# Performance work log

Measured on AMD Instinct MI355X. Metric: run time of the kernel, lower is better.

The kernel has to match this reference:

```python
import jax, jax.numpy as jnp
import numpy as np

# Segment geometry (from init_kwargs): modes ['u','uv','v'] -> out_v = alpha * x_u @ W_uv
U = 128
V = 128
IN_OFF = [0, 128, 256, 384]
W_OFF = [k * U * V for k in range(8)]          # [0,16384,...,114688]
OUT_OFF = [0, 128, 256, 384]
IN_STRIDE = 512
OUT_STRIDE = 512
W_STRIDE = 8 * U * V                           # 131072
# (in_seg, w_seg, out_seg, coefficient)
PATHS = [(0, 0, 0, 1.0), (1, 1, 1, 1.0), (2, 2, 2, 1.0), (3, 3, 3, 1.0),
         (0, 4, 1, 0.5), (1, 5, 2, 0.5), (2, 6, 3, 0.5), (3, 7, 0, 0.5)]
B = 32768
E = 4  # num_embeddings (experts)


def setup_inputs() -> dict:
    key = jax.random.key(0)
    k1, k2, k3 = jax.random.split(key, 3)
    tensor_in = jax.random.normal(k1, (B, IN_STRIDE), dtype=jnp.float32)
    tensor_w = jax.random.normal(k2, (E, W_STRIDE), dtype=jnp.float32)
    tensor_w_id = jax.random.randint(k3, (B,), 0, E, dtype=jnp.int32)
    return {"tensor_in": tensor_in, "tensor_w": tensor_w, "tensor_w_id": tensor_w_id}


def _batch_linear(tensor_in, tensor_w, tensor_w_id):
    """Segmented path-indexed grouped linear (cuEquivariance BatchLinear fwd).

    tensor_in: [B, IN_STRIDE]; tensor_w: [E, W_STRIDE]; tensor_w_id: [B] int in [0,E).
    For each path (i, j, k, alpha):
        out[b, OUT_OFF[k]:+V] += alpha * x[b, IN_OFF[i]:+U] @ W[w_id[b], seg j].reshape(U, V)
    """
    nb = tensor_in.shape[0]
    ne = tensor_w.shape[0]
    onehot = jax.nn.one_hot(tensor_w_id, ne, dtype=tensor_in.dtype)  # [B, E]
    out = jnp.zeros((nb, OUT_STRIDE), dtype=tensor_in.dtype)
    for (i, j, k, a) in PATHS:
        x = tensor_in[:, IN_OFF[i]:IN_OFF[i] + U]                    # [B, U]
        w_seg = tensor_w[:, W_OFF[j]:W_OFF[j] + U * V].reshape(ne, U, V)
        # masked per-expert dense GEMMs (small fixed expert count)
        y = jnp.zeros((nb, V), dtype=tensor_in.dtype)
        for e in range(ne):
            y = y + onehot[:, e:e + 1] * (x @ w_seg[e])              # [B, V]
        out = out.at[:, OUT_OFF[k]:OUT_OFF[k] + V].add(a * y)
    return out


def reference(tensor_in, tensor_w, tensor_w_id):
    return _batch_linear(tensor_in, tensor_w, tensor_w_id)
```

## Files before the change

### kernel.cpp

```cpp
#include <hip/hip_runtime.h>
#include <stdint.h>

#define U 128
#define V 128
#define IN_STRIDE 512
#define OUT_STRIDE 512
#define NEXP 4
#define W_STRIDE (8 * U * V)
#define B_ROWS 32768

#define WS_WSHUF 0
#define WS_PERM (1048576)
#define WS_COUNTS (1048576 + 131072)
#define WS_CURS (WS_COUNTS + 16)

typedef __bf16 bf16x8 __attribute__((ext_vector_type(8)));
typedef float f32x16 __attribute__((ext_vector_type(16)));
typedef unsigned int u32x4 __attribute__((ext_vector_type(4)));
typedef unsigned int u32x2 __attribute__((ext_vector_type(2)));

static __device__ __forceinline__ unsigned short f2bf(float f) {
    unsigned int u = __builtin_bit_cast(unsigned int, f);
    u += 0x7FFFu + ((u >> 16) & 1u);
    return (unsigned short)(u >> 16);
}

__global__ void prep_kernel(const float* __restrict__ w, const int* __restrict__ wid,
                            unsigned short* __restrict__ wshuf, int* __restrict__ counts) {
    int blk = blockIdx.x;
    if (blk < 256) {
        int t = blk * 256 + threadIdx.x;
        int lane = t & 63;
        int kt = (t >> 6) & 7;
        int nt = (t >> 9) & 3;
        int s  = (t >> 11) & 7;
        int e  = (t >> 14) & 3;
        int kbase = kt * 16 + ((lane >> 5) << 3);
        int n = nt * 32 + (lane & 31);
        const float* src = w + (size_t)e * W_STRIDE + (size_t)s * (U * V) + n;
        float sc = (s >= 4) ? 0.5f : 1.0f;
        __attribute__((aligned(16))) unsigned short o[8];
#pragma unroll
        for (int j = 0; j < 8; j++) o[j] = f2bf(src[(size_t)(kbase + j) * V] * sc);
        *(u32x4*)(wshuf + (size_t)t * 8) = *(const u32x4*)o;
    } else {
        __shared__ int lc[4];
        if (threadIdx.x < 4) lc[threadIdx.x] = 0;
        __syncthreads();
        int b = (blk - 256) * 256 + threadIdx.x;
        atomicAdd(&lc[wid[b]], 1);
        __syncthreads();
        if (threadIdx.x < 4) atomicAdd(&counts[threadIdx.x], lc[threadIdx.x]);
    }
}

__global__ void scatter_kernel(const int* __restrict__ wid, const int* __restrict__ counts,
                               int* __restrict__ cursors, int* __restrict__ perm) {
    __shared__ int lcnt[4], lbase[4];
    int tid = threadIdx.x;
    if (tid < 4) lcnt[tid] = 0;
    __syncthreads();
    int b = blockIdx.x * 256 + tid;
    int e = wid[b];
    int r = atomicAdd(&lcnt[e], 1);
    __syncthreads();
    if (tid < 4) lbase[tid] = atomicAdd(&cursors[tid], lcnt[tid]);
    __syncthreads();
    int off = 0;
#pragma unroll
    for (int i = 0; i < 4; i++)
        if (i < e) off += counts[i];
    perm[off + lbase[e] + r] = b;
}

__global__ __launch_bounds__(512) void gemm_kernel(
        const float* __restrict__ x, const unsigned short* __restrict__ wshuf,
        const int* __restrict__ counts, const int* __restrict__ perm,
        float* __restrict__ out) {
    int e = blockIdx.y;
    int tile = blockIdx.x;
    int c0 = counts[0], c1 = counts[1], c2 = counts[2], c3 = counts[3];
    int cnt = (e == 0) ? c0 : (e == 1) ? c1 : (e == 2) ? c2 : c3;
    int start = 0;
    if (e > 0) start += c0;
    if (e > 1) start += c1;
    if (e > 2) start += c2;
    if (tile * 64 >= cnt) return;
    int rows = cnt - tile * 64;
    if (rows > 64) rows = 64;
    int tstart = start + tile * 64;

    __shared__ unsigned short lds[64 * 512];

    int t = threadIdx.x;

    {
        int r = t >> 3;
        int g = t & 7;
        bool valid = (r < rows);
        int row_g = valid ? perm[tstart + r] : 0;
        const float* xr = x + (size_t)row_g * IN_STRIDE;
#pragma unroll
        for (int i = 0; i < 16; i++) {
            int c = g * 4 + i * 32;
            float4 v = valid ? *(const float4*)(xr + c) : make_float4(0.f, 0.f, 0.f, 0.f);
            __attribute__((aligned(8))) unsigned short h[4];
            h[0] = f2bf(v.x); h[1] = f2bf(v.y); h[2] = f2bf(v.z); h[3] = f2bf(v.w);
            int off = r * 512 + ((((c >> 3) ^ (r & 7))) << 3) + (c & 7);
            *(u32x2*)(lds + off) = *(const u32x2*)h;
        }
    }
    __syncthreads();

    int w = t >> 6;
    int lane = t & 63;
    int kout = w >> 1;
    int nhalf = w & 1;

    f32x16 acc00 = {}, acc01 = {}, acc10 = {}, acc11 = {};

    int xb[2]; int sg[2];
    xb[0] = kout;            sg[0] = kout;
    xb[1] = (kout + 3) & 3;  sg[1] = xb[1] + 4;

    const int m0 = lane & 31;
    const int khalf = (lane >> 5) << 3;
    const int rowswz = (m0 & 7);

#pragma unroll
    for (int c = 0; c < 2; c++) {
        int colbase = xb[c] * 128;
        const unsigned short* wseg =
            wshuf + (((size_t)(e * 8 + sg[c]) * 4 + nhalf * 2) * 8) * 64 * 8;
#pragma unroll
        for (int kt = 0; kt < 8; kt++) {
            int kabs = colbase + kt * 16 + khalf;
            int packoff = (((kabs >> 3) ^ rowswz) << 3);
            bf16x8 a0 = __builtin_bit_cast(bf16x8, *(const u32x4*)(lds + m0 * 512 + packoff));
            bf16x8 a1 = __builtin_bit_cast(bf16x8, *(const u32x4*)(lds + (m0 + 32) * 512 + packoff));
            bf16x8 b0 = __builtin_bit_cast(bf16x8, *(const u32x4*)(wseg + ((size_t)(kt) * 64 + lane) * 8));
            bf16x8 b1 = __builtin_bit_cast(bf16x8, *(const u32x4*)(wseg + ((size_t)(8 + kt) * 64 + lane) * 8));
            acc00 = __builtin_amdgcn_mfma_f32_32x32x16_bf16(a0, b0, acc00, 0, 0, 0);
            acc01 = __builtin_amdgcn_mfma_f32_32x32x16_bf16(a0, b1, acc01, 0, 0, 0);
            acc10 = __builtin_amdgcn_mfma_f32_32x32x16_bf16(a1, b0, acc10, 0, 0, 0);
            acc11 = __builtin_amdgcn_mfma_f32_32x32x16_bf16(a1, b1, acc11, 0, 0, 0);
        }
    }

    int colb = kout * 128 + nhalf * 64 + (lane & 31);
    int rh = (lane >> 5) << 2;
#pragma unroll
    for (int q = 0; q < 4; q++) {
#pragma unroll
        for (int d = 0; d < 4; d++) {
            int reg = q * 4 + d;
            int rl0 = d + 8 * q + rh;
            if (rl0 < rows) {
                int rg = perm[tstart + rl0];
                out[(size_t)rg * OUT_STRIDE + colb]      = acc00[reg];
                out[(size_t)rg * OUT_STRIDE + colb + 32] = acc01[reg];
            }
            int rl1 = rl0 + 32;
            if (rl1 < rows) {
                int rg = perm[tstart + rl1];
                out[(size_t)rg * OUT_STRIDE + colb]      = acc10[reg];
                out[(size_t)rg * OUT_STRIDE + colb + 32] = acc11[reg];
            }
        }
    }
}

extern "C" void kernel_launch(void* const* d_in, const int* in_sizes, int n_in,
                              void* d_out, int out_size, void* d_ws, size_t ws_size,
                              hipStream_t stream) {
    const float* x = (const float*)d_in[0];
    const float* w = (const float*)d_in[1];
    const int* wid = (const int*)d_in[2];
    float* out = (float*)d_out;

    char* ws = (char*)d_ws;
    unsigned short* wshuf = (unsigned short*)(ws + WS_WSHUF);
    int* perm = (int*)(ws + WS_PERM);
    int* counts = (int*)(ws + WS_COUNTS);
    int* cursors = (int*)(ws + WS_CURS);

    hipMemsetAsync(counts, 0, 32, stream);
    prep_kernel<<<384, 256, 0, stream>>>(w, wid, wshuf, counts);
    scatter_kernel<<<128, 256, 0, stream>>>(wid, counts, cursors, perm);
    gemm_kernel<<<dim3(512, 4), 512, 0, stream>>>(x, wshuf, counts, perm, out);
}
```

Baseline: 151.6 us.

## Fuse scatter into prep kernel and retile GEMM to 32-row expert tiles

Merges the permutation scatter into the prep kernel by giving each expert a fixed NB-sized region in the perm buffer, which removes the separate counts pass and one kernel launch. The GEMM now uses 32-row tiles on a compact 1D grid mapped across experts, caches the permutation indices in shared memory, and halves LDS usage. In exchange, weight reuse per block drops, so more weight traffic goes through L2.

```diff
diff --git a/kernel.cpp b/kernel.cpp
--- a/kernel.cpp
+++ b/kernel.cpp
@@ -5,14 +5,12 @@
 #define V 128
 #define IN_STRIDE 512
 #define OUT_STRIDE 512
-#define NEXP 4
 #define W_STRIDE (8 * U * V)
-#define B_ROWS 32768
+#define NB 32768
 
 #define WS_WSHUF 0
-#define WS_PERM (1048576)
-#define WS_COUNTS (1048576 + 131072)
-#define WS_CURS (WS_COUNTS + 16)
+#define WS_PERM  (1 << 20)
+#define WS_CURS  ((1 << 20) + (1 << 19))
 
 typedef __bf16 bf16x8 __attribute__((ext_vector_type(8)));
 typedef float f32x16 __attribute__((ext_vector_type(16)));
@@ -26,7 +24,8 @@
 }
 
 __global__ void prep_kernel(const float* __restrict__ w, const int* __restrict__ wid,
-                            unsigned short* __restrict__ wshuf, int* __restrict__ counts) {
+                            unsigned short* __restrict__ wshuf, int* __restrict__ cursors,
+                            int* __restrict__ perm) {
     int blk = blockIdx.x;
     if (blk < 256) {
         int t = blk * 256 + threadIdx.x;
@@ -44,65 +43,55 @@
         for (int j = 0; j < 8; j++) o[j] = f2bf(src[(size_t)(kbase + j) * V] * sc);
         *(u32x4*)(wshuf + (size_t)t * 8) = *(const u32x4*)o;
     } else {
-        __shared__ int lc[4];
-        if (threadIdx.x < 4) lc[threadIdx.x] = 0;
+        __shared__ int lcnt[4], lbase[4];
+        int tid = threadIdx.x;
+        if (tid < 4) lcnt[tid] = 0;
         __syncthreads();
-        int b = (blk - 256) * 256 + threadIdx.x;
-        atomicAdd(&lc[wid[b]], 1);
+        int b = (blk - 256) * 256 + tid;
+        int e = wid[b];
+        int r = atomicAdd(&lcnt[e], 1);
         __syncthreads();
-        if (threadIdx.x < 4) atomicAdd(&counts[threadIdx.x], lc[threadIdx.x]);
+        if (tid < 4) lbase[tid] = atomicAdd(&cursors[tid], lcnt[tid]);
+        __syncthreads();
+        perm[e * NB + lbase[e] + r] = b;
     }
-}
-
-__global__ void scatter_kernel(const int* __restrict__ wid, const int* __restrict__ counts,
-                               int* __restrict__ cursors, int* __restrict__ perm) {
-    __shared__ int lcnt[4], lbase[4];
-    int tid = threadIdx.x;
-    if (tid < 4) lcnt[tid] = 0;
-    __syncthreads();
-    int b = blockIdx.x * 256 + tid;
-    int e = wid[b];
-    int r = atomicAdd(&lcnt[e], 1);
-    __syncthreads();
-    if (tid < 4) lbase[tid] = atomicAdd(&cursors[tid], lcnt[tid]);
-    __syncthreads();
-    int off = 0;
-#pragma unroll
-    for (int i = 0; i < 4; i++)
-        if (i < e) off += counts[i];
-    perm[off + lbase[e] + r] = b;
 }
 
 __global__ __launch_bounds__(512) void gemm_kernel(
         const float* __restrict__ x, const unsigned short* __restrict__ wshuf,
-        const int* __restrict__ counts, const int* __restrict__ perm,
+        const int* __restrict__ cursors, const int* __restrict__ perm,
         float* __restrict__ out) {
-    int e = blockIdx.y;
-    int tile = blockIdx.x;
-    int c0 = counts[0], c1 = counts[1], c2 = counts[2], c3 = counts[3];
-    int cnt = (e == 0) ? c0 : (e == 1) ? c1 : (e == 2) ? c2 : c3;
-    int start = 0;
-    if (e > 0) start += c0;
-    if (e > 1) start += c1;
-    if (e > 2) start += c2;
-    if (tile * 64 >= cnt) return;
-    int rows = cnt - tile * 64;
-    if (rows > 64) rows = 64;
-    int tstart = start + tile * 64;
+    int c4_0 = cursors[0], c4_1 = cursors[1], c4_2 = cursors[2], c4_3 = cursors[3];
+    int cnts[4] = {c4_0, c4_1, c4_2, c4_3};
+    int g = blockIdx.x;
+    int e = -1, tile = 0, acc = 0;
+#pragma unroll
+    for (int i = 0; i < 4; i++) {
+        int te = (cnts[i] + 31) >> 5;
+        if (e < 0 && g < acc + te) { e = i; tile = g - acc; }
+        acc += te;
+    }
+    if (e < 0) return;
+    int cnt = cnts[e];
+    int rows = cnt - tile * 32;
+    if (rows > 32) rows = 32;
+    int tbase = e * NB + tile * 32;
 
-    __shared__ unsigned short lds[64 * 512];
+    __shared__ unsigned short lds[32 * 512];
+    __shared__ int s_perm[32];
 
     int t = threadIdx.x;
 
     {
-        int r = t >> 3;
-        int g = t & 7;
+        int r = t >> 4;
+        int gg = t & 15;
         bool valid = (r < rows);
-        int row_g = valid ? perm[tstart + r] : 0;
+        int row_g = valid ? perm[tbase + r] : 0;
+        if (gg == 0) s_perm[r] = row_g;
         const float* xr = x + (size_t)row_g * IN_STRIDE;
 #pragma unroll
-        for (int i = 0; i < 16; i++) {
-            int c = g * 4 + i * 32;
+        for (int i = 0; i < 8; i++) {
+            int c = gg * 4 + i * 64;
             float4 v = valid ? *(const float4*)(xr + c) : make_float4(0.f, 0.f, 0.f, 0.f);
             __attribute__((aligned(8))) unsigned short h[4];
             h[0] = f2bf(v.x); h[1] = f2bf(v.y); h[2] = f2bf(v.z); h[3] = f2bf(v.w);
@@ -117,7 +106,7 @@
     int kout = w >> 1;
     int nhalf = w & 1;
 
-    f32x16 acc00 = {}, acc01 = {}, acc10 = {}, acc11 = {};
+    f32x16 acc0 = {}, acc1 = {};
 
     int xb[2]; int sg[2];
     xb[0] = kout;            sg[0] = kout;
@@ -137,13 +126,10 @@
             int kabs = colbase + kt * 16 + khalf;
             int packoff = (((kabs >> 3) ^ rowswz) << 3);
             bf16x8 a0 = __builtin_bit_cast(bf16x8, *(const u32x4*)(lds + m0 * 512 + packoff));
-            bf16x8 a1 = __builtin_bit_cast(bf16x8, *(const u32x4*)(lds + (m0 + 32) * 512 + packoff));
             bf16x8 b0 = __builtin_bit_cast(bf16x8, *(const u32x4*)(wseg + ((size_t)(kt) * 64 + lane) * 8));
             bf16x8 b1 = __builtin_bit_cast(bf16x8, *(const u32x4*)(wseg + ((size_t)(8 + kt) * 64 + lane) * 8));
-            acc00 = __builtin_amdgcn_mfma_f32_32x32x16_bf16(a0, b0, acc00, 0, 0, 0);
-            acc01 = __builtin_amdgcn_mfma_f32_32x32x16_bf16(a0, b1, acc01, 0, 0, 0);
-            acc10 = __builtin_amdgcn_mfma_f32_32x32x16_bf16(a1, b0, acc10, 0, 0, 0);
-            acc11 = __builtin_amdgcn_mfma_f32_32x32x16_bf16(a1, b1, acc11, 0, 0, 0);
+            acc0 = __builtin_amdgcn_mfma_f32_32x32x16_bf16(a0, b0, acc0, 0, 0, 0);
+            acc1 = __builtin_amdgcn_mfma_f32_32x32x16_bf16(a0, b1, acc1, 0, 0, 0);
         }
     }
 
@@ -154,17 +140,11 @@
 #pragma unroll
         for (int d = 0; d < 4; d++) {
             int reg = q * 4 + d;
-            int rl0 = d + 8 * q + rh;
-            if (rl0 < rows) {
-                int rg = perm[tstart + rl0];
-                out[(size_t)rg * OUT_STRIDE + colb]      = acc00[reg];
-                out[(size_t)rg * OUT_STRIDE + colb + 32] = acc01[reg];
-            }
-            int rl1 = rl0 + 32;
-            if (rl1 < rows) {
-                int rg = perm[tstart + rl1];
-                out[(size_t)rg * OUT_STRIDE + colb]      = acc10[reg];
-                out[(size_t)rg * OUT_STRIDE + colb + 32] = acc11[reg];
+            int rl = d + 8 * q + rh;
+            if (rl < rows) {
+                int rg = s_perm[rl];
+                out[(size_t)rg * OUT_STRIDE + colb]      = acc0[reg];
+                out[(size_t)rg * OUT_STRIDE + colb + 32] = acc1[reg];
             }
         }
     }
@@ -181,11 +161,9 @@
     char* ws = (char*)d_ws;
     unsigned short* wshuf = (unsigned short*)(ws + WS_WSHUF);
     int* perm = (int*)(ws + WS_PERM);
-    int* counts = (int*)(ws + WS_COUNTS);
     int* cursors = (int*)(ws + WS_CURS);
 
-    hipMemsetAsync(counts, 0, 32, stream);
-    prep_kernel<<<384, 256, 0, stream>>>(w, wid, wshuf, counts);
-    scatter_kernel<<<128, 256, 0, stream>>>(wid, counts, cursors, perm);
-    gemm_kernel<<<dim3(512, 4), 512, 0, stream>>>(x, wshuf, counts, perm, out);
+    hipMemsetAsync(cursors, 0, 16, stream);
+    prep_kernel<<<384, 256, 0, stream>>>(w, wid, wshuf, cursors, perm);
+    gemm_kernel<<<1027, 512, 0, stream>>>(x, wshuf, cursors, perm, out);
 }
```

New measurement: 136.2 us. -10.2%, faster.
